# Optimization experiments

Measured on AMD Instinct MI355X. Metric: run time of the kernel, lower is better.

Reference implementation:

```python
import jax, jax.numpy as jnp
import numpy as np

N_NODES = 50000
N_EDGES = 800000
DIM = 128
HEADS = 8
DK = DIM // HEADS  # 16
SQRT_DK = float(np.sqrt(DK))


def setup_inputs() -> dict:
    key = jax.random.key(0)
    ks = jax.random.split(key, 12)
    inp = {
        "h": jax.random.normal(ks[0], (N_NODES, DIM), jnp.float32),
        "src": jax.random.randint(ks[1], (N_EDGES,), 0, N_NODES, jnp.int32),
        "dst": jax.random.randint(ks[2], (N_EDGES,), 0, N_NODES, jnp.int32),
        "Wk": jax.random.normal(ks[3], (DIM, DIM), jnp.float32) / np.sqrt(DIM),
        "bk": jnp.zeros((DIM,), jnp.float32),
        "Wq": jax.random.normal(ks[4], (DIM, DIM), jnp.float32) / np.sqrt(DIM),
        "bq": jnp.zeros((DIM,), jnp.float32),
        "Wv": jax.random.normal(ks[5], (DIM, DIM), jnp.float32) / np.sqrt(DIM),
        "bv": jnp.zeros((DIM,), jnp.float32),
        "Wa": jax.random.normal(ks[6], (DIM, DIM), jnp.float32) / np.sqrt(DIM),
        "ba": jnp.zeros((DIM,), jnp.float32),
        "rel_att": jax.random.normal(ks[7], (HEADS, DK, DK), jnp.float32) / np.sqrt(DK),
        "rel_msg": jax.random.normal(ks[8], (HEADS, DK, DK), jnp.float32) / np.sqrt(DK),
        "rel_pri": jnp.ones((HEADS,), jnp.float32),
        "skip": jnp.ones((1,), jnp.float32),
    }
    return inp


def reference(h, src, dst, Wk, bk, Wq, bq, Wv, bv, Wa, ba, rel_att, rel_msg, rel_pri, skip):
    N = h.shape[0]
    # node-level projections -> [N, H, d_k]
    k = (h @ Wk + bk).reshape(N, HEADS, DK)
    q = (h @ Wq + bq).reshape(N, HEADS, DK)
    v = (h @ Wv + bv).reshape(N, HEADS, DK)
    # relation-specific transforms
    k = jnp.einsum('nhi,hij->nhj', k, rel_att)
    v = jnp.einsum('nhi,hij->nhj', v, rel_msg)
    # per-edge score: dot(q[dst], k[src]) over d_k -> [E, H]
    score = jnp.einsum('ehd,ehd->eh', q[dst], k[src]) * rel_pri / SQRT_DK
    # segment softmax over destination nodes (edge_softmax, norm_by='dst')
    smax = jax.ops.segment_max(score, dst, num_segments=N)  # [N, H]
    e = jnp.exp(score - smax[dst])
    ssum = jax.ops.segment_sum(e, dst, num_segments=N)  # [N, H]
    attn = e / ssum[dst]  # [E, H]
    # weighted scatter-sum of messages: sum_e v[src_e] * attn_e -> [N, H, d_k]
    m = v[src] * attn[:, :, None]
    t = jax.ops.segment_sum(m, dst, num_segments=N).reshape(N, DIM)
    # target-specific aggregation (dropout in eval mode = identity, use_norm=False)
    trans_out = t @ Wa + ba
    alpha = jax.nn.sigmoid(skip)  # [1], broadcasts
    new_h = trans_out * alpha + h * (1.0 - alpha)
    return new_h
```

## Files before the change

kernel.cpp:

```cpp
#include <hip/hip_runtime.h>
#include <stdint.h>

#define NN 50000
#define NE 800000

typedef __bf16 v8bf __attribute__((ext_vector_type(8)));
typedef float  v4f  __attribute__((ext_vector_type(4)));
typedef unsigned short v8us __attribute__((ext_vector_type(8)));

#define EXP2F(x) __builtin_amdgcn_exp2f(x)

__device__ __forceinline__ float bf2f(unsigned short u) {
    return __uint_as_float(((unsigned)u) << 16);
}
__device__ __forceinline__ unsigned short f2bf(float f) {
    unsigned u = __float_as_uint(f);
    u += 0x7FFFu + ((u >> 16) & 1u);
    return (unsigned short)(u >> 16);
}
__device__ __forceinline__ float ldf(const void* p, size_t i, int isb) {
    return isb ? bf2f(((const unsigned short*)p)[i]) : ((const float*)p)[i];
}

__global__ __launch_bounds__(128) void k_prep(
    const void* __restrict__ Wq, const void* __restrict__ bq,
    const void* __restrict__ Wk, const void* __restrict__ bk,
    const void* __restrict__ Wv, const void* __restrict__ bv,
    const void* __restrict__ Wa, const void* __restrict__ ba,
    const void* __restrict__ rel_att, const void* __restrict__ rel_msg,
    const void* __restrict__ rel_pri, const int* __restrict__ dst,
    unsigned* __restrict__ CNTP,
    int* __restrict__ FLAG, unsigned short* __restrict__ WTb,
    float* __restrict__ BC)
{
    int b = blockIdx.x;
    int j = threadIdx.x;
    if (b >= 512) {
        int e = (b - 512) * 128 + j;
        atomicAdd(&CNTP[(unsigned)dst[e] << 4], 1u);
        return;
    }
    const unsigned rp0 = ((const unsigned*)rel_pri)[0];
    const int isb = ((rp0 & 0xFFFFu) != 0u) ? 1 : 0;
    int m = b >> 7;
    int i = b & 127;
    if (b == 0 && j == 0) FLAG[0] = isb;
    if (m == 0) {
        WTb[((size_t)(0 * 128 + j)) * 128 + i] = f2bf(ldf(Wq, i * 128 + j, isb));
        if (i == 0) BC[j] = ldf(bq, j, isb);
    } else if (m == 3) {
        WTb[((size_t)(3 * 128 + j)) * 128 + i] = f2bf(ldf(Wa, i * 128 + j, isb));
        if (i == 0) BC[3 * 128 + j] = ldf(ba, j, isb);
    } else {
        const void* W    = (m == 1) ? Wk : Wv;
        const void* bias = (m == 1) ? bk : bv;
        const void* R    = (m == 1) ? rel_att : rel_msg;
        int hh = j >> 4, jj = j & 15;
        float scale = (m == 1) ? ldf(rel_pri, hh, isb) * 0.25f : 1.0f;
        float acc = 0.f, bacc = 0.f;
        #pragma unroll
        for (int l = 0; l < 16; ++l) {
            float r = ldf(R, hh * 256 + l * 16 + jj, isb);
            acc  += ldf(W, i * 128 + hh * 16 + l, isb) * r;
            bacc += ldf(bias, hh * 16 + l, isb) * r;
        }
        WTb[((size_t)(m * 128 + j)) * 128 + i] = f2bf(acc * scale);
        if (i == 0) BC[m * 128 + j] = bacc * scale;
    }
}

__global__ __launch_bounds__(256) void k_qkv(
    const void* __restrict__ h, const unsigned short* __restrict__ WTb,
    const float* __restrict__ BC, const int* __restrict__ FLAG,
    unsigned short* __restrict__ Qb, unsigned short* __restrict__ KVb)
{
    __shared__ __align__(16) unsigned short Ah[64][136];
    __shared__ __align__(16) unsigned short Bh[128][136];
    const int isb = FLAG[0];
    const int tid = threadIdx.x;
    const int rowBase = blockIdx.x * 64;

    if (isb) {
        #pragma unroll
        for (int i = 0; i < 4; ++i) {
            int lin = tid + i * 256;
            int row = lin >> 4, kc = (lin & 15) * 8;
            int gr = rowBase + row;
            uint4 u = make_uint4(0, 0, 0, 0);
            if (gr < NN) u = *(const uint4*)((const unsigned short*)h + (size_t)gr * 128 + kc);
            *(uint4*)&Ah[row][kc] = u;
        }
    } else {
        #pragma unroll
        for (int i = 0; i < 8; ++i) {
            int lin = tid + i * 256;
            int row = lin >> 5, c4 = (lin & 31) * 4;
            int gr = rowBase + row;
            ushort4 o = make_ushort4(0, 0, 0, 0);
            if (gr < NN) {
                float4 f = *(const float4*)((const float*)h + (size_t)gr * 128 + c4);
                o.x = f2bf(f.x); o.y = f2bf(f.y); o.z = f2bf(f.z); o.w = f2bf(f.w);
            }
            *(ushort4*)&Ah[row][c4] = o;
        }
    }

    const int w = tid >> 6, l = tid & 63;
    const int lr = l & 15, q = l >> 4;
    v4f accK[8];

    for (int m = 0; m < 3; ++m) {
        if (m) __syncthreads();
        #pragma unroll
        for (int i = 0; i < 8; ++i) {
            int lin = tid + i * 256;
            int col = lin >> 4, kc = (lin & 15) * 8;
            uint4 u = *(const uint4*)(WTb + ((size_t)(m * 128 + col)) * 128 + kc);
            *(uint4*)&Bh[col][kc] = u;
        }
        __syncthreads();

        v4f acc[8];
        #pragma unroll
        for (int nt = 0; nt < 8; ++nt) {
            float bj = BC[m * 128 + nt * 16 + lr];
            acc[nt] = (v4f){bj, bj, bj, bj};
        }
        #pragma unroll
        for (int kk = 0; kk < 4; ++kk) {
            v8bf a = *(const v8bf*)&Ah[w * 16 + lr][kk * 32 + q * 8];
            #pragma unroll
            for (int nt = 0; nt < 8; ++nt) {
                v8bf b = *(const v8bf*)&Bh[nt * 16 + lr][kk * 32 + q * 8];
                acc[nt] = __builtin_amdgcn_mfma_f32_16x16x32_bf16(a, b, acc[nt], 0, 0, 0);
            }
        }
        if (m == 0) {
            #pragma unroll
            for (int nt = 0; nt < 8; ++nt)
                #pragma unroll
                for (int r = 0; r < 4; ++r) {
                    int row = rowBase + w * 16 + q * 4 + r;
                    if (row < NN)
                        Qb[(size_t)row * 128 + nt * 16 + lr] = f2bf(acc[nt][r]);
                }
        } else if (m == 1) {
            #pragma unroll
            for (int nt = 0; nt < 8; ++nt) accK[nt] = acc[nt];
        } else {
            #pragma unroll
            for (int nt = 0; nt < 8; ++nt)
                #pragma unroll
                for (int r = 0; r < 4; ++r) {
                    int row = rowBase + w * 16 + q * 4 + r;
                    if (row < NN) {
                        ushort2 kv;
                        kv.x = f2bf(accK[nt][r]);
                        kv.y = f2bf(acc[nt][r]);
                        *(ushort2*)&KVb[(size_t)row * 256 + (nt * 16 + lr) * 2] = kv;
                    }
                }
        }
    }
}

#define SCB 512
#define NSB 98
__global__ __launch_bounds__(SCB) void k_scan(
    const unsigned* __restrict__ CNTP, unsigned* __restrict__ RPS,
    unsigned* __restrict__ BSUM, unsigned* __restrict__ BOFF,
    unsigned* __restrict__ DONE)
{
    __shared__ unsigned sh[SCB];
    __shared__ int lastFlag;
    int tid = threadIdx.x;
    int g = blockIdx.x * SCB + tid;
    unsigned v = (g < NN) ? CNTP[(size_t)g << 4] : 0u;
    sh[tid] = v;
    __syncthreads();
    #pragma unroll
    for (int off = 1; off < SCB; off <<= 1) {
        unsigned t = 0;
        if (tid >= off) t = sh[tid - off];
        __syncthreads();
        if (tid >= off) sh[tid] += t;
        __syncthreads();
    }
    if (g < NN) RPS[g] = sh[tid] - v;
    if (tid == SCB - 1) atomicExch(&BSUM[blockIdx.x], sh[tid]);
    __syncthreads();
    if (tid == 0) {
        __threadfence();
        lastFlag = (atomicAdd(DONE, 1u) == NSB - 1);
    }
    __syncthreads();
    if (!lastFlag) return;

    unsigned bv = (tid < NSB) ? atomicAdd(&BSUM[tid], 0u) : 0u;
    sh[tid] = bv;
    __syncthreads();
    #pragma unroll
    for (int off = 1; off < SCB; off <<= 1) {
        unsigned t = 0;
        if (tid >= off) t = sh[tid - off];
        __syncthreads();
        if (tid >= off) sh[tid] += t;
        __syncthreads();
    }
    if (tid < NSB) BOFF[tid] = sh[tid] - bv;
}

__global__ __launch_bounds__(256) void k_fill(
    const int* __restrict__ src, const int* __restrict__ dst,
    const unsigned* __restrict__ RPS, const unsigned* __restrict__ BOFF,
    unsigned* __restrict__ CURP, int* __restrict__ ESRC)
{
    int e = blockIdx.x * 256 + threadIdx.x;
    int d = dst[e];
    int pos = (int)atomicAdd(&CURP[(unsigned)d << 4], 1u);
    ESRC[(int)(RPS[d] + BOFF[d >> 9]) + pos] = src[e];
}

__global__ __launch_bounds__(256) void k_attn(
    const unsigned* __restrict__ RPS, const unsigned* __restrict__ BOFF,
    const int* __restrict__ ESRC,
    const unsigned short* __restrict__ Qb, const unsigned short* __restrict__ KVb,
    unsigned short* __restrict__ Tb)
{
    int d = (blockIdx.x * 256 + threadIdx.x) >> 6;
    int lane = threadIdx.x & 63;
    int hl = lane >> 5;
    int sub = lane & 31;
    int beg = (int)(RPS[d] + BOFF[d >> 9]);
    int end = (d == NN - 1) ? NE : (int)(RPS[d + 1] + BOFF[(d + 1) >> 9]);
    const float LOG2E = 1.4426950408889634f;

    const ushort4 qu = *(const ushort4*)(Qb + (size_t)d * 128 + sub * 4);
    float q0 = bf2f(qu.x) * LOG2E, q1 = bf2f(qu.y) * LOG2E;
    float q2 = bf2f(qu.z) * LOG2E, q3 = bf2f(qu.w) * LOG2E;

    float s = 0.f, o0 = 0.f, o1 = 0.f, o2 = 0.f, o3 = 0.f;
    for (int j = beg; j < end; j += 8) {
        v8us kv[4];
        int valid[4];
        #pragma unroll
        for (int t = 0; t < 4; ++t) {
            int idx = j + 2 * t + hl;
            valid[t] = idx < end;
            int sid = ESRC[valid[t] ? idx : end - 1];
            kv[t] = *(const v8us*)(KVb + (size_t)sid * 256 + sub * 8);
        }
        #pragma unroll
        for (int t = 0; t < 4; ++t) {
            float p = q0 * bf2f(kv[t][0]) + q1 * bf2f(kv[t][2])
                    + q2 * bf2f(kv[t][4]) + q3 * bf2f(kv[t][6]);
            p += __shfl_xor(p, 1);
            p += __shfl_xor(p, 2);
            float w = valid[t] ? EXP2F(p) : 0.f;
            s  += w;
            o0 += w * bf2f(kv[t][1]);
            o1 += w * bf2f(kv[t][3]);
            o2 += w * bf2f(kv[t][5]);
            o3 += w * bf2f(kv[t][7]);
        }
    }
    s  += __shfl_xor(s, 32);
    o0 += __shfl_xor(o0, 32);
    o1 += __shfl_xor(o1, 32);
    o2 += __shfl_xor(o2, 32);
    o3 += __shfl_xor(o3, 32);
    float r = (s > 0.f) ? (1.0f / s) : 0.f;
    if (hl == 0) {
        ushort4 o;
        o.x = f2bf(o0 * r); o.y = f2bf(o1 * r);
        o.z = f2bf(o2 * r); o.w = f2bf(o3 * r);
        *(ushort4*)(Tb + (size_t)d * 128 + sub * 4) = o;
    }
}

__global__ __launch_bounds__(256) void k_final_m(
    const unsigned short* __restrict__ Tb, const unsigned short* __restrict__ WTb,
    const float* __restrict__ BC, const void* __restrict__ h,
    const void* __restrict__ skip, const int* __restrict__ FLAG,
    void* __restrict__ out)
{
    __shared__ __align__(16) unsigned short Ah[64][136];
    __shared__ __align__(16) unsigned short Bh[128][136];
    const int isb = FLAG[0];
    const int tid = threadIdx.x;
    const int rowBase = blockIdx.x * 64;

    #pragma unroll
    for (int i = 0; i < 4; ++i) {
        int lin = tid + i * 256;
        int row = lin >> 4, kc = (lin & 15) * 8;
        int gr = rowBase + row;
        uint4 u = make_uint4(0, 0, 0, 0);
        if (gr < NN) u = *(const uint4*)(Tb + (size_t)gr * 128 + kc);
        *(uint4*)&Ah[row][kc] = u;
    }
    #pragma unroll
    for (int i = 0; i < 8; ++i) {
        int lin = tid + i * 256;
        int col = lin >> 4, kc = (lin & 15) * 8;
        uint4 u = *(const uint4*)(WTb + ((size_t)(3 * 128 + col)) * 128 + kc);
        *(uint4*)&Bh[col][kc] = u;
    }
    __syncthreads();

    const int w = tid >> 6, l = tid & 63;
    const int lr = l & 15, q = l >> 4;
    v4f acc[8];
    #pragma unroll
    for (int nt = 0; nt < 8; ++nt) {
        float bj = BC[3 * 128 + nt * 16 + lr];
        acc[nt] = (v4f){bj, bj, bj, bj};
    }
    #pragma unroll
    for (int kk = 0; kk < 4; ++kk) {
        v8bf a = *(const v8bf*)&Ah[w * 16 + lr][kk * 32 + q * 8];
        #pragma unroll
        for (int nt = 0; nt < 8; ++nt) {
            v8bf b = *(const v8bf*)&Bh[nt * 16 + lr][kk * 32 + q * 8];
            acc[nt] = __builtin_amdgcn_mfma_f32_16x16x32_bf16(a, b, acc[nt], 0, 0, 0);
        }
    }
    float skipv = ldf(skip, 0, isb);
    float alpha = 1.0f / (1.0f + __expf(-skipv));
    float beta = 1.0f - alpha;
    #pragma unroll
    for (int nt = 0; nt < 8; ++nt) {
        #pragma unroll
        for (int r = 0; r < 4; ++r) {
            int row = rowBase + w * 16 + q * 4 + r;
            if (row < NN) {
                size_t off = (size_t)row * 128 + nt * 16 + lr;
                float hv = ldf(h, off, isb);
                float o = alpha * acc[nt][r] + beta * hv;
                if (isb) ((unsigned short*)out)[off] = f2bf(o);
                else     ((float*)out)[off] = o;
            }
        }
    }
}

extern "C" void kernel_launch(void* const* d_in, const int* in_sizes, int n_in,
                              void* d_out, int out_size, void* d_ws, size_t ws_size,
                              hipStream_t stream)
{
    const void* h  = d_in[0];
    const int* src = (const int*)d_in[1];
    const int* dst = (const int*)d_in[2];
    const void* Wk = d_in[3];
    const void* bk = d_in[4];
    const void* Wq = d_in[5];
    const void* bq = d_in[6];
    const void* Wv = d_in[7];
    const void* bv = d_in[8];
    const void* Wa = d_in[9];
    const void* ba = d_in[10];
    const void* rel_att = d_in[11];
    const void* rel_msg = d_in[12];
    const void* rel_pri = d_in[13];
    const void* skip    = d_in[14];

    float* F = (float*)d_ws;
    int* FLAG      = (int*)F;
    float* BC      = F + 16;
    unsigned short* WTb = (unsigned short*)(BC + 512);
    unsigned* CNTP = (unsigned*)((float*)(BC + 512) + 32768);
    unsigned* CURP = CNTP + 800000;
    unsigned* DONE = CURP + 800000;
    unsigned* RPS  = DONE + 16;
    unsigned* BSUM = RPS + 50048;
    unsigned* BOFF = BSUM + 128;
    unsigned short* Tb = (unsigned short*)(BOFF + 128);
    int* ESRC      = (int*)(Tb + (size_t)NN * 128);
    unsigned short* Qb  = (unsigned short*)(ESRC + NE);
    unsigned short* KVb = Qb + (size_t)NN * 128;

    (void)hipMemsetAsync(CNTP, 0, (800000 + 800000 + 16) * sizeof(unsigned), stream);

    k_prep<<<512 + 6250, 128, 0, stream>>>(Wq, bq, Wk, bk, Wv, bv, Wa, ba,
                                           rel_att, rel_msg, rel_pri, dst, CNTP,
                                           FLAG, WTb, BC);
    k_qkv<<<782, 256, 0, stream>>>(h, WTb, BC, FLAG, Qb, KVb);
    k_scan<<<NSB, SCB, 0, stream>>>(CNTP, RPS, BSUM, BOFF, DONE);
    k_fill<<<NE / 256, 256, 0, stream>>>(src, dst, RPS, BOFF, CURP, ESRC);
    k_attn<<<(NN * 64) / 256, 256, 0, stream>>>(RPS, BOFF, ESRC, Qb, KVb, Tb);
    k_final_m<<<782, 256, 0, stream>>>(Tb, WTb, BC, h, skip, FLAG, d_out);
}
```

Baseline: 281.2 us.

## Fuse scan into QKV kernel, vectorize fill, prefetch attention gathers

The separate scan kernel is folded into extra blocks of the QKV projection kernel, so the CSR prefix scan runs alongside the GEMM and one launch goes away. Those scan blocks also zero CURP, which shrinks the memset. The fill kernel now handles four edges per thread with int4 loads. The attention loop double-buffers its edge gathers, issuing the next 8 edges' loads before computing on the current ones, which raises register pressure.

```diff
diff --git a/kernel.cpp b/kernel.cpp
--- a/kernel.cpp
+++ b/kernel.cpp
@@ -69,15 +69,67 @@
     }
 }
 
-__global__ __launch_bounds__(256) void k_qkv(
+#define NSB 98
+__global__ __launch_bounds__(256) void k_qkvscan(
     const void* __restrict__ h, const unsigned short* __restrict__ WTb,
     const float* __restrict__ BC, const int* __restrict__ FLAG,
-    unsigned short* __restrict__ Qb, unsigned short* __restrict__ KVb)
+    unsigned short* __restrict__ Qb, unsigned short* __restrict__ KVb,
+    const unsigned* __restrict__ CNTP, unsigned* __restrict__ CURP,
+    unsigned* __restrict__ RPS, unsigned* __restrict__ BSUM,
+    unsigned* __restrict__ BOFF, unsigned* __restrict__ DONE)
 {
     __shared__ __align__(16) unsigned short Ah[64][136];
     __shared__ __align__(16) unsigned short Bh[128][136];
+    __shared__ int lastFlag;
+    const int tid = threadIdx.x;
+
+    if (blockIdx.x >= 782) {
+        unsigned* shs = (unsigned*)&Ah[0][0];
+        int sb = blockIdx.x - 782;
+        int g0 = sb * 512 + tid * 2, g1 = g0 + 1;
+        unsigned v0 = (g0 < NN) ? CNTP[(size_t)g0 << 4] : 0u;
+        unsigned v1 = (g1 < NN) ? CNTP[(size_t)g1 << 4] : 0u;
+        if (g0 < NN) CURP[(size_t)g0 << 4] = 0u;
+        if (g1 < NN) CURP[(size_t)g1 << 4] = 0u;
+        unsigned pv = v0 + v1;
+        shs[tid] = pv;
+        __syncthreads();
+        #pragma unroll
+        for (int off = 1; off < 256; off <<= 1) {
+            unsigned t = 0;
+            if (tid >= off) t = shs[tid - off];
+            __syncthreads();
+            if (tid >= off) shs[tid] += t;
+            __syncthreads();
+        }
+        unsigned excl = shs[tid] - pv;
+        if (g0 < NN) RPS[g0] = excl;
+        if (g1 < NN) RPS[g1] = excl + v0;
+        if (tid == 255) atomicExch(&BSUM[sb], shs[255]);
+        __syncthreads();
+        if (tid == 0) {
+            __threadfence();
+            lastFlag = (atomicAdd(DONE, 1u) == NSB - 1);
+        }
+        __syncthreads();
+        if (!lastFlag) return;
+        unsigned bv = (tid < NSB) ? atomicAdd(&BSUM[tid], 0u) : 0u;
+        __syncthreads();
+        shs[tid] = bv;
+        __syncthreads();
+        #pragma unroll
+        for (int off = 1; off < 256; off <<= 1) {
+            unsigned t = 0;
+            if (tid >= off) t = shs[tid - off];
+            __syncthreads();
+            if (tid >= off) shs[tid] += t;
+            __syncthreads();
+        }
+        if (tid < NSB) BOFF[tid] = shs[tid] - bv;
+        return;
+    }
+
     const int isb = FLAG[0];
-    const int tid = threadIdx.x;
     const int rowBase = blockIdx.x * 64;
 
     if (isb) {
@@ -164,61 +216,24 @@
     }
 }
 
-#define SCB 512
-#define NSB 98
-__global__ __launch_bounds__(SCB) void k_scan(
-    const unsigned* __restrict__ CNTP, unsigned* __restrict__ RPS,
-    unsigned* __restrict__ BSUM, unsigned* __restrict__ BOFF,
-    unsigned* __restrict__ DONE)
-{
-    __shared__ unsigned sh[SCB];
-    __shared__ int lastFlag;
-    int tid = threadIdx.x;
-    int g = blockIdx.x * SCB + tid;
-    unsigned v = (g < NN) ? CNTP[(size_t)g << 4] : 0u;
-    sh[tid] = v;
-    __syncthreads();
-    #pragma unroll
-    for (int off = 1; off < SCB; off <<= 1) {
-        unsigned t = 0;
-        if (tid >= off) t = sh[tid - off];
-        __syncthreads();
-        if (tid >= off) sh[tid] += t;
-        __syncthreads();
-    }
-    if (g < NN) RPS[g] = sh[tid] - v;
-    if (tid == SCB - 1) atomicExch(&BSUM[blockIdx.x], sh[tid]);
-    __syncthreads();
-    if (tid == 0) {
-        __threadfence();
-        lastFlag = (atomicAdd(DONE, 1u) == NSB - 1);
-    }
-    __syncthreads();
-    if (!lastFlag) return;
-
-    unsigned bv = (tid < NSB) ? atomicAdd(&BSUM[tid], 0u) : 0u;
-    sh[tid] = bv;
-    __syncthreads();
-    #pragma unroll
-    for (int off = 1; off < SCB; off <<= 1) {
-        unsigned t = 0;
-        if (tid >= off) t = sh[tid - off];
-        __syncthreads();
-        if (tid >= off) sh[tid] += t;
-        __syncthreads();
-    }
-    if (tid < NSB) BOFF[tid] = sh[tid] - bv;
-}
-
 __global__ __launch_bounds__(256) void k_fill(
     const int* __restrict__ src, const int* __restrict__ dst,
     const unsigned* __restrict__ RPS, const unsigned* __restrict__ BOFF,
     unsigned* __restrict__ CURP, int* __restrict__ ESRC)
 {
-    int e = blockIdx.x * 256 + threadIdx.x;
-    int d = dst[e];
-    int pos = (int)atomicAdd(&CURP[(unsigned)d << 4], 1u);
-    ESRC[(int)(RPS[d] + BOFF[d >> 9]) + pos] = src[e];
+    int t = blockIdx.x * 256 + threadIdx.x;
+    if (t >= NE / 4) return;
+    int e = t * 4;
+    const int4 d4 = *(const int4*)(dst + e);
+    const int4 s4 = *(const int4*)(src + e);
+    unsigned p0 = atomicAdd(&CURP[(size_t)(unsigned)d4.x << 4], 1u);
+    unsigned p1 = atomicAdd(&CURP[(size_t)(unsigned)d4.y << 4], 1u);
+    unsigned p2 = atomicAdd(&CURP[(size_t)(unsigned)d4.z << 4], 1u);
+    unsigned p3 = atomicAdd(&CURP[(size_t)(unsigned)d4.w << 4], 1u);
+    ESRC[(int)(RPS[d4.x] + BOFF[d4.x >> 9] + p0)] = s4.x;
+    ESRC[(int)(RPS[d4.y] + BOFF[d4.y >> 9] + p1)] = s4.y;
+    ESRC[(int)(RPS[d4.z] + BOFF[d4.z >> 9] + p2)] = s4.z;
+    ESRC[(int)(RPS[d4.w] + BOFF[d4.w >> 9] + p3)] = s4.w;
 }
 
 __global__ __launch_bounds__(256) void k_attn(
@@ -240,29 +255,43 @@
     float q2 = bf2f(qu.z) * LOG2E, q3 = bf2f(qu.w) * LOG2E;
 
     float s = 0.f, o0 = 0.f, o1 = 0.f, o2 = 0.f, o3 = 0.f;
+    v8us kvA[4]; int vA[4];
+    if (beg < end) {
+        #pragma unroll
+        for (int t = 0; t < 4; ++t) {
+            int idx = beg + 2 * t + hl;
+            vA[t] = idx < end;
+            int sid = ESRC[vA[t] ? idx : end - 1];
+            kvA[t] = *(const v8us*)(KVb + (size_t)sid * 256 + sub * 8);
+        }
+    }
     for (int j = beg; j < end; j += 8) {
-        v8us kv[4];
-        int valid[4];
+        v8us kvB[4]; int vB[4] = {0, 0, 0, 0};
+        int jn = j + 8;
+        if (jn < end) {
+            #pragma unroll
+            for (int t = 0; t < 4; ++t) {
+                int idx = jn + 2 * t + hl;
+                vB[t] = idx < end;
+                int sid = ESRC[vB[t] ? idx : end - 1];
+                kvB[t] = *(const v8us*)(KVb + (size_t)sid * 256 + sub * 8);
+            }
+        }
         #pragma unroll
         for (int t = 0; t < 4; ++t) {
-            int idx = j + 2 * t + hl;
-            valid[t] = idx < end;
-            int sid = ESRC[valid[t] ? idx : end - 1];
-            kv[t] = *(const v8us*)(KVb + (size_t)sid * 256 + sub * 8);
-        }
-        #pragma unroll
-        for (int t = 0; t < 4; ++t) {
-            float p = q0 * bf2f(kv[t][0]) + q1 * bf2f(kv[t][2])
-                    + q2 * bf2f(kv[t][4]) + q3 * bf2f(kv[t][6]);
+            float p = q0 * bf2f(kvA[t][0]) + q1 * bf2f(kvA[t][2])
+                    + q2 * bf2f(kvA[t][4]) + q3 * bf2f(kvA[t][6]);
             p += __shfl_xor(p, 1);
             p += __shfl_xor(p, 2);
-            float w = valid[t] ? EXP2F(p) : 0.f;
+            float w = vA[t] ? EXP2F(p) : 0.f;
             s  += w;
-            o0 += w * bf2f(kv[t][1]);
-            o1 += w * bf2f(kv[t][3]);
-            o2 += w * bf2f(kv[t][5]);
-            o3 += w * bf2f(kv[t][7]);
-        }
+            o0 += w * bf2f(kvA[t][1]);
+            o1 += w * bf2f(kvA[t][3]);
+            o2 += w * bf2f(kvA[t][5]);
+            o3 += w * bf2f(kvA[t][7]);
+        }
+        #pragma unroll
+        for (int t = 0; t < 4; ++t) { kvA[t] = kvB[t]; vA[t] = vB[t]; }
     }
     s  += __shfl_xor(s, 32);
     o0 += __shfl_xor(o0, 32);
@@ -369,9 +398,9 @@
     float* BC      = F + 16;
     unsigned short* WTb = (unsigned short*)(BC + 512);
     unsigned* CNTP = (unsigned*)((float*)(BC + 512) + 32768);
-    unsigned* CURP = CNTP + 800000;
-    unsigned* DONE = CURP + 800000;
-    unsigned* RPS  = DONE + 16;
+    unsigned* DONE = CNTP + 800000;
+    unsigned* CURP = DONE + 16;
+    unsigned* RPS  = CURP + 800000;
     unsigned* BSUM = RPS + 50048;
     unsigned* BOFF = BSUM + 128;
     unsigned short* Tb = (unsigned short*)(BOFF + 128);
@@ -379,14 +408,14 @@
     unsigned short* Qb  = (unsigned short*)(ESRC + NE);
     unsigned short* KVb = Qb + (size_t)NN * 128;
 
-    (void)hipMemsetAsync(CNTP, 0, (800000 + 800000 + 16) * sizeof(unsigned), stream);
+    (void)hipMemsetAsync(CNTP, 0, (800000 + 16) * sizeof(unsigned), stream);
 
     k_prep<<<512 + 6250, 128, 0, stream>>>(Wq, bq, Wk, bk, Wv, bv, Wa, ba,
                                            rel_att, rel_msg, rel_pri, dst, CNTP,
                                            FLAG, WTb, BC);
-    k_qkv<<<782, 256, 0, stream>>>(h, WTb, BC, FLAG, Qb, KVb);
-    k_scan<<<NSB, SCB, 0, stream>>>(CNTP, RPS, BSUM, BOFF, DONE);
-    k_fill<<<NE / 256, 256, 0, stream>>>(src, dst, RPS, BOFF, CURP, ESRC);
+    k_qkvscan<<<782 + NSB, 256, 0, stream>>>(h, WTb, BC, FLAG, Qb, KVb,
+                                             CNTP, CURP, RPS, BSUM, BOFF, DONE);
+    k_fill<<<(NE / 4 + 255) / 256, 256, 0, stream>>>(src, dst, RPS, BOFF, CURP, ESRC);
     k_attn<<<(NN * 64) / 256, 256, 0, stream>>>(RPS, BOFF, ESRC, Qb, KVb, Tb);
     k_final_m<<<782, 256, 0, stream>>>(Tb, WTb, BC, h, skip, FLAG, d_out);
 }
```

Measured after the change: 296.7 us. +5.5%, slower.
